# Kernel optimization log

Measured on AMD Instinct MI355X. Metric: run time of the kernel, lower is better.

Reference implementation:

```python
import jax, jax.numpy as jnp
import numpy as np
from jax import lax

EPS = 1e-7  # keras K.epsilon()
DN = ('NHWC', 'HWIO', 'NHWC')


def _box_avg(z, k):
    """Depthwise k x k box filter with SAME padding, scaled by 1/(k*k*C).
    Matches tf.nn.depthwise_conv2d with a ones/(k*k*C) kernel, implemented
    separably (two 1D convs) for efficiency."""
    C = z.shape[-1]
    scale = 1.0 / (k * k * C)  # note: keras code divides by full kernel size incl. C
    kh = jnp.ones((k, 1, 1, C), z.dtype)
    kw = jnp.ones((1, k, 1, C), z.dtype)
    z = lax.conv_general_dilated(z, kh, (1, 1), 'SAME',
                                 dimension_numbers=DN, feature_group_count=C)
    z = lax.conv_general_dilated(z, kw, (1, 1), 'SAME',
                                 dimension_numbers=DN, feature_group_count=C)
    return z * scale


def setup_inputs() -> dict:
    key = jax.random.key(0)
    x = jax.random.normal(key, (8, 1024, 1024, 2), dtype=jnp.float32)
    return {"x": x, "filter_size": 61}


def reference(x, filter_size):
    k = int(filter_size)
    # norm_method == 'std':
    out = x - _box_avg(x, k)                       # local mean-subtract
    c1 = _box_avg(out, k)
    c2 = _box_avg(out * out, k)
    std = jnp.sqrt(c2 - c1 * c1) + EPS             # local window std
    return out / std
```

## Files before the change

### kernel.cpp

```cpp
#include <hip/hip_runtime.h>
#include <math.h>

#define NB 8
#define HH 1024
#define WW 1024
#define CC 2
#define RAD 30
#define KS 61
#define ROWSZ (WW * CC)
#define IMGSZ (HH * ROWSZ)
#define STR4 (ROWSZ / 4)
#define NCOL4 (NB * STR4)
#define VSEGH 32
#define VNSEG (HH / VSEGH)
#define EPSV 1e-7f
#define SCALEV (1.0f / (float)(KS * KS * CC))
#define PDW (WW + WW / 8)
#define PD(i) ((i) + ((i) >> 3))

__device__ __forceinline__ float4 f4add(float4 a, float4 b) {
    return make_float4(a.x + b.x, a.y + b.y, a.z + b.z, a.w + b.w);
}
__device__ __forceinline__ float4 f4sub(float4 a, float4 b) {
    return make_float4(a.x - b.x, a.y - b.y, a.z - b.z, a.w - b.w);
}
__device__ __forceinline__ float4 f4fma(float4 a, float4 b, float4 c) {
    return make_float4(fmaf(a.x, b.x, c.x), fmaf(a.y, b.y, c.y),
                       fmaf(a.z, b.z, c.z), fmaf(a.w, b.w, c.w));
}

__global__ __launch_bounds__(256) void vbox_kernel(const float* __restrict__ in,
                                                   float* __restrict__ out) {
    int tid = blockIdx.x * 256 + threadIdx.x;
    int col = tid & (NCOL4 - 1);
    int seg = tid >> 12;
    int n = col >> 9;
    int w4 = col & (STR4 - 1);
    const float4* ip = (const float4*)(in + (size_t)n * IMGSZ) + w4;
    float4* op = (float4*)(out + (size_t)n * IMGSZ) + w4;
    int h0 = seg * VSEGH;
    float4 S = make_float4(0.f, 0.f, 0.f, 0.f);
    int lo = h0 - RAD; if (lo < 0) lo = 0;
    int hiex = h0 + RAD;
    int h = lo;
    for (; h + 4 <= hiex; h += 4) {
        float4 v0 = ip[(h + 0) * STR4];
        float4 v1 = ip[(h + 1) * STR4];
        float4 v2 = ip[(h + 2) * STR4];
        float4 v3 = ip[(h + 3) * STR4];
        S = f4add(S, f4add(f4add(v0, v1), f4add(v2, v3)));
    }
    for (; h < hiex; ++h) S = f4add(S, ip[h * STR4]);

    if (seg != 0 && seg != VNSEG - 1) {
        for (int ho = h0; ho < h0 + VSEGH; ho += 4) {
            float4 a0 = ip[(ho + 0 + RAD) * STR4];
            float4 a1 = ip[(ho + 1 + RAD) * STR4];
            float4 a2 = ip[(ho + 2 + RAD) * STR4];
            float4 a3 = ip[(ho + 3 + RAD) * STR4];
            float4 b0 = ip[(ho + 0 - RAD) * STR4];
            float4 b1 = ip[(ho + 1 - RAD) * STR4];
            float4 b2 = ip[(ho + 2 - RAD) * STR4];
            float4 b3 = ip[(ho + 3 - RAD) * STR4];
            S = f4add(S, a0); op[(ho + 0) * STR4] = S; S = f4sub(S, b0);
            S = f4add(S, a1); op[(ho + 1) * STR4] = S; S = f4sub(S, b1);
            S = f4add(S, a2); op[(ho + 2) * STR4] = S; S = f4sub(S, b2);
            S = f4add(S, a3); op[(ho + 3) * STR4] = S; S = f4sub(S, b3);
        }
    } else {
        const float4 Z = make_float4(0.f, 0.f, 0.f, 0.f);
        for (int ho = h0; ho < h0 + VSEGH; ho += 4) {
            float4 a[4], b[4];
            #pragma unroll
            for (int i = 0; i < 4; ++i) {
                int ha = ho + i + RAD;
                a[i] = (ha < HH) ? ip[ha * STR4] : Z;
            }
            #pragma unroll
            for (int i = 0; i < 4; ++i) {
                int hb = ho + i - RAD;
                b[i] = (hb >= 0) ? ip[hb * STR4] : Z;
            }
            #pragma unroll
            for (int i = 0; i < 4; ++i) {
                S = f4add(S, a[i]);
                op[(ho + i) * STR4] = S;
                S = f4sub(S, b[i]);
            }
        }
    }
}

__global__ __launch_bounds__(256) void vbox2_kernel(const float* __restrict__ in,
                                                    float* __restrict__ o1,
                                                    float* __restrict__ o2) {
    int tid = blockIdx.x * 256 + threadIdx.x;
    int col = tid & (NCOL4 - 1);
    int seg = tid >> 12;
    int n = col >> 9;
    int w4 = col & (STR4 - 1);
    const float4* ip = (const float4*)(in + (size_t)n * IMGSZ) + w4;
    float4* p1 = (float4*)(o1 + (size_t)n * IMGSZ) + w4;
    float4* p2 = (float4*)(o2 + (size_t)n * IMGSZ) + w4;
    int h0 = seg * VSEGH;
    float4 S = make_float4(0.f, 0.f, 0.f, 0.f);
    float4 Q = make_float4(0.f, 0.f, 0.f, 0.f);
    int lo = h0 - RAD; if (lo < 0) lo = 0;
    int hiex = h0 + RAD;
    int h = lo;
    for (; h + 4 <= hiex; h += 4) {
        float4 v0 = ip[(h + 0) * STR4];
        float4 v1 = ip[(h + 1) * STR4];
        float4 v2 = ip[(h + 2) * STR4];
        float4 v3 = ip[(h + 3) * STR4];
        S = f4add(S, f4add(f4add(v0, v1), f4add(v2, v3)));
        Q = f4fma(v0, v0, Q); Q = f4fma(v1, v1, Q);
        Q = f4fma(v2, v2, Q); Q = f4fma(v3, v3, Q);
    }
    for (; h < hiex; ++h) {
        float4 v = ip[h * STR4];
        S = f4add(S, v); Q = f4fma(v, v, Q);
    }

    if (seg != 0 && seg != VNSEG - 1) {
        for (int ho = h0; ho < h0 + VSEGH; ho += 4) {
            float4 a0 = ip[(ho + 0 + RAD) * STR4];
            float4 a1 = ip[(ho + 1 + RAD) * STR4];
            float4 a2 = ip[(ho + 2 + RAD) * STR4];
            float4 a3 = ip[(ho + 3 + RAD) * STR4];
            float4 b0 = ip[(ho + 0 - RAD) * STR4];
            float4 b1 = ip[(ho + 1 - RAD) * STR4];
            float4 b2 = ip[(ho + 2 - RAD) * STR4];
            float4 b3 = ip[(ho + 3 - RAD) * STR4];
            S = f4add(S, a0); Q = f4fma(a0, a0, Q);
            p1[(ho + 0) * STR4] = S; p2[(ho + 0) * STR4] = Q;
            S = f4sub(S, b0); Q = make_float4(fmaf(-b0.x, b0.x, Q.x), fmaf(-b0.y, b0.y, Q.y), fmaf(-b0.z, b0.z, Q.z), fmaf(-b0.w, b0.w, Q.w));
            S = f4add(S, a1); Q = f4fma(a1, a1, Q);
            p1[(ho + 1) * STR4] = S; p2[(ho + 1) * STR4] = Q;
            S = f4sub(S, b1); Q = make_float4(fmaf(-b1.x, b1.x, Q.x), fmaf(-b1.y, b1.y, Q.y), fmaf(-b1.z, b1.z, Q.z), fmaf(-b1.w, b1.w, Q.w));
            S = f4add(S, a2); Q = f4fma(a2, a2, Q);
            p1[(ho + 2) * STR4] = S; p2[(ho + 2) * STR4] = Q;
            S = f4sub(S, b2); Q = make_float4(fmaf(-b2.x, b2.x, Q.x), fmaf(-b2.y, b2.y, Q.y), fmaf(-b2.z, b2.z, Q.z), fmaf(-b2.w, b2.w, Q.w));
            S = f4add(S, a3); Q = f4fma(a3, a3, Q);
            p1[(ho + 3) * STR4] = S; p2[(ho + 3) * STR4] = Q;
            S = f4sub(S, b3); Q = make_float4(fmaf(-b3.x, b3.x, Q.x), fmaf(-b3.y, b3.y, Q.y), fmaf(-b3.z, b3.z, Q.z), fmaf(-b3.w, b3.w, Q.w));
        }
    } else {
        const float4 Z = make_float4(0.f, 0.f, 0.f, 0.f);
        for (int ho = h0; ho < h0 + VSEGH; ho += 4) {
            float4 a[4], b[4];
            #pragma unroll
            for (int i = 0; i < 4; ++i) {
                int ha = ho + i + RAD;
                a[i] = (ha < HH) ? ip[ha * STR4] : Z;
            }
            #pragma unroll
            for (int i = 0; i < 4; ++i) {
                int hb = ho + i - RAD;
                b[i] = (hb >= 0) ? ip[hb * STR4] : Z;
            }
            #pragma unroll
            for (int i = 0; i < 4; ++i) {
                S = f4add(S, a[i]); Q = f4fma(a[i], a[i], Q);
                p1[(ho + i) * STR4] = S; p2[(ho + i) * STR4] = Q;
                S = f4sub(S, b[i]);
                Q = make_float4(fmaf(-b[i].x, b[i].x, Q.x), fmaf(-b[i].y, b[i].y, Q.y),
                                fmaf(-b[i].z, b[i].z, Q.z), fmaf(-b[i].w, b[i].w, Q.w));
            }
        }
    }
}

__device__ inline float wave_incl_scan(float v) {
    int lane = threadIdx.x & 63;
    #pragma unroll
    for (int d = 1; d < 64; d <<= 1) {
        float o = __shfl_up(v, d, 64);
        if (lane >= d) v += o;
    }
    return v;
}

__global__ __launch_bounds__(256) void hbox_sub_kernel(const float* __restrict__ vsum,
                                                       const float* __restrict__ x,
                                                       float* __restrict__ out) {
    __shared__ float ch[2][PDW];
    __shared__ float wtot[4];
    int t = threadIdx.x;
    size_t g = (size_t)blockIdx.x * ROWSZ;
    const float4* vrow = (const float4*)(vsum + g);
    #pragma unroll
    for (int i = 0; i < 2; ++i) {
        int j = t + 256 * i;
        float4 v = vrow[j];
        ch[0][PD(2 * j)] = v.x;     ch[1][PD(2 * j)] = v.y;
        ch[0][PD(2 * j + 1)] = v.z; ch[1][PD(2 * j + 1)] = v.w;
    }
    __syncthreads();
    int c = t >> 7, j = t & 127, base = j * 8;
    float v[8]; float run = 0.f;
    #pragma unroll
    for (int i = 0; i < 8; ++i) { run += ch[c][PD(base + i)]; v[i] = run; }
    float incl = wave_incl_scan(run);
    int wid = t >> 6;
    if ((t & 63) == 63) wtot[wid] = incl;
    __syncthreads();
    float off = incl - run;
    if (wid & 1) off += wtot[wid - 1];
    #pragma unroll
    for (int i = 0; i < 8; ++i) ch[c][PD(base + i)] = off + v[i];
    __syncthreads();
    const float4* xrow = (const float4*)(x + g);
    float4* orow = (float4*)(out + g);
    #pragma unroll
    for (int i = 0; i < 2; ++i) {
        int jj = t + 256 * i;
        int w0 = 2 * jj, w1 = 2 * jj + 1;
        int hi0 = w0 + RAD; if (hi0 > WW - 1) hi0 = WW - 1;
        int hi1 = w1 + RAD; if (hi1 > WW - 1) hi1 = WW - 1;
        int lo0 = w0 - RAD - 1, lo1 = w1 - RAD - 1;
        float s00 = ch[0][PD(hi0)], s10 = ch[1][PD(hi0)];
        if (lo0 >= 0) { s00 -= ch[0][PD(lo0)]; s10 -= ch[1][PD(lo0)]; }
        float s01 = ch[0][PD(hi1)], s11 = ch[1][PD(hi1)];
        if (lo1 >= 0) { s01 -= ch[0][PD(lo1)]; s11 -= ch[1][PD(lo1)]; }
        float4 xv = xrow[jj];
        float4 o;
        o.x = xv.x - SCALEV * s00; o.y = xv.y - SCALEV * s10;
        o.z = xv.z - SCALEV * s01; o.w = xv.w - SCALEV * s11;
        orow[jj] = o;
    }
}

__global__ __launch_bounds__(256) void hbox_final_kernel(const float* __restrict__ s1v,
                                                         const float* __restrict__ s2v,
                                                         float* __restrict__ out) {
    __shared__ float ch[4][PDW];
    int t = threadIdx.x;
    size_t g = (size_t)blockIdx.x * ROWSZ;
    const float4* arow = (const float4*)(s1v + g);
    const float4* brow = (const float4*)(s2v + g);
    #pragma unroll
    for (int i = 0; i < 2; ++i) {
        int j = t + 256 * i;
        float4 a = arow[j];
        ch[0][PD(2 * j)] = a.x;     ch[1][PD(2 * j)] = a.y;
        ch[0][PD(2 * j + 1)] = a.z; ch[1][PD(2 * j + 1)] = a.w;
        float4 b = brow[j];
        ch[2][PD(2 * j)] = b.x;     ch[3][PD(2 * j)] = b.y;
        ch[2][PD(2 * j + 1)] = b.z; ch[3][PD(2 * j + 1)] = b.w;
    }
    __syncthreads();
    int a = t >> 6, j = t & 63, base = j * 16;
    float v[16]; float run = 0.f;
    #pragma unroll
    for (int i = 0; i < 16; ++i) { run += ch[a][PD(base + i)]; v[i] = run; }
    float incl = wave_incl_scan(run);
    float off = incl - run;
    #pragma unroll
    for (int i = 0; i < 16; ++i) ch[a][PD(base + i)] = off + v[i];
    __syncthreads();
    float4* orow = (float4*)(out + g);
    #pragma unroll
    for (int i = 0; i < 2; ++i) {
        int jj = t + 256 * i;
        int w0 = 2 * jj, w1 = 2 * jj + 1;
        int hi0 = w0 + RAD; if (hi0 > WW - 1) hi0 = WW - 1;
        int hi1 = w1 + RAD; if (hi1 > WW - 1) hi1 = WW - 1;
        int lo0 = w0 - RAD - 1, lo1 = w1 - RAD - 1;
        float s1a = ch[0][PD(hi0)], s1b = ch[1][PD(hi0)];
        float s2a = ch[2][PD(hi0)], s2b = ch[3][PD(hi0)];
        if (lo0 >= 0) {
            s1a -= ch[0][PD(lo0)]; s1b -= ch[1][PD(lo0)];
            s2a -= ch[2][PD(lo0)]; s2b -= ch[3][PD(lo0)];
        }
        float s1c = ch[0][PD(hi1)], s1d = ch[1][PD(hi1)];
        float s2c = ch[2][PD(hi1)], s2d = ch[3][PD(hi1)];
        if (lo1 >= 0) {
            s1c -= ch[0][PD(lo1)]; s1d -= ch[1][PD(lo1)];
            s2c -= ch[2][PD(lo1)]; s2d -= ch[3][PD(lo1)];
        }
        float4 ov = orow[jj];
        float c1, c2, var;
        float4 r;
        c1 = SCALEV * s1a; c2 = SCALEV * s2a; var = c2 - c1 * c1;
        r.x = ov.x / (sqrtf(fmaxf(var, 0.f)) + EPSV);
        c1 = SCALEV * s1b; c2 = SCALEV * s2b; var = c2 - c1 * c1;
        r.y = ov.y / (sqrtf(fmaxf(var, 0.f)) + EPSV);
        c1 = SCALEV * s1c; c2 = SCALEV * s2c; var = c2 - c1 * c1;
        r.z = ov.z / (sqrtf(fmaxf(var, 0.f)) + EPSV);
        c1 = SCALEV * s1d; c2 = SCALEV * s2d; var = c2 - c1 * c1;
        r.w = ov.w / (sqrtf(fmaxf(var, 0.f)) + EPSV);
        orow[jj] = r;
    }
}

extern "C" void kernel_launch(void* const* d_in, const int* in_sizes, int n_in,
                              void* d_out, int out_size, void* d_ws, size_t ws_size,
                              hipStream_t stream) {
    const float* x = (const float*)d_in[0];
    float* out = (float*)d_out;
    float* wsf = (float*)d_ws;
    float* V1 = wsf;
    float* V3 = wsf + (size_t)NB * IMGSZ;

    vbox_kernel<<<(NCOL4 * VNSEG) / 256, 256, 0, stream>>>(x, V1);
    hbox_sub_kernel<<<NB * HH, 256, 0, stream>>>(V1, x, out);
    vbox2_kernel<<<(NCOL4 * VNSEG) / 256, 256, 0, stream>>>(out, V1, V3);
    hbox_final_kernel<<<NB * HH, 256, 0, stream>>>(V1, V3, out);
}
```

Baseline: 251.7 us.

## Fuse horizontal box passes and move second vertical box into final normalization

Reorders the separable filters so the second stage does the horizontal box sums of both out and out² in the same block that computes out, writing horizontal sums to workspace. A new vertical kernel then box-sums those and applies the std normalization directly, removing one kernel and the separate final pass. It also adds software prefetching of the next rows in the vertical loops and sets launch bounds occupancy hints. The trade-off is extra global writes of two horizontal-sum buffers and two streams read in the vertical pass.

```diff
diff --git a/kernel.cpp b/kernel.cpp
--- a/kernel.cpp
+++ b/kernel.cpp
@@ -4,17 +4,16 @@
 #define NB 8
 #define HH 1024
 #define WW 1024
-#define CC 2
 #define RAD 30
 #define KS 61
-#define ROWSZ (WW * CC)
+#define ROWSZ 2048
 #define IMGSZ (HH * ROWSZ)
-#define STR4 (ROWSZ / 4)
+#define STR4 512
 #define NCOL4 (NB * STR4)
 #define VSEGH 32
 #define VNSEG (HH / VSEGH)
 #define EPSV 1e-7f
-#define SCALEV (1.0f / (float)(KS * KS * CC))
+#define SCALEV (1.0f / (float)(KS * KS * 2))
 #define PDW (WW + WW / 8)
 #define PD(i) ((i) + ((i) >> 3))
 
@@ -24,13 +23,9 @@
 __device__ __forceinline__ float4 f4sub(float4 a, float4 b) {
     return make_float4(a.x - b.x, a.y - b.y, a.z - b.z, a.w - b.w);
 }
-__device__ __forceinline__ float4 f4fma(float4 a, float4 b, float4 c) {
-    return make_float4(fmaf(a.x, b.x, c.x), fmaf(a.y, b.y, c.y),
-                       fmaf(a.z, b.z, c.z), fmaf(a.w, b.w, c.w));
-}
-
-__global__ __launch_bounds__(256) void vbox_kernel(const float* __restrict__ in,
-                                                   float* __restrict__ out) {
+
+__global__ __launch_bounds__(256, 2) void vbox_kernel(const float* __restrict__ in,
+                                                      float* __restrict__ out) {
     int tid = blockIdx.x * 256 + threadIdx.x;
     int col = tid & (NCOL4 - 1);
     int seg = tid >> 12;
@@ -38,38 +33,43 @@
     int w4 = col & (STR4 - 1);
     const float4* ip = (const float4*)(in + (size_t)n * IMGSZ) + w4;
     float4* op = (float4*)(out + (size_t)n * IMGSZ) + w4;
-    int h0 = seg * VSEGH;
+    int h0 = seg * VSEGH, hend = h0 + VSEGH;
     float4 S = make_float4(0.f, 0.f, 0.f, 0.f);
     int lo = h0 - RAD; if (lo < 0) lo = 0;
-    int hiex = h0 + RAD;
     int h = lo;
-    for (; h + 4 <= hiex; h += 4) {
+    for (; h + 4 <= h0 + RAD; h += 4) {
         float4 v0 = ip[(h + 0) * STR4];
         float4 v1 = ip[(h + 1) * STR4];
         float4 v2 = ip[(h + 2) * STR4];
         float4 v3 = ip[(h + 3) * STR4];
         S = f4add(S, f4add(f4add(v0, v1), f4add(v2, v3)));
     }
-    for (; h < hiex; ++h) S = f4add(S, ip[h * STR4]);
+    for (; h < h0 + RAD; ++h) S = f4add(S, ip[h * STR4]);
 
     if (seg != 0 && seg != VNSEG - 1) {
-        for (int ho = h0; ho < h0 + VSEGH; ho += 4) {
-            float4 a0 = ip[(ho + 0 + RAD) * STR4];
-            float4 a1 = ip[(ho + 1 + RAD) * STR4];
-            float4 a2 = ip[(ho + 2 + RAD) * STR4];
-            float4 a3 = ip[(ho + 3 + RAD) * STR4];
-            float4 b0 = ip[(ho + 0 - RAD) * STR4];
-            float4 b1 = ip[(ho + 1 - RAD) * STR4];
-            float4 b2 = ip[(ho + 2 - RAD) * STR4];
-            float4 b3 = ip[(ho + 3 - RAD) * STR4];
-            S = f4add(S, a0); op[(ho + 0) * STR4] = S; S = f4sub(S, b0);
-            S = f4add(S, a1); op[(ho + 1) * STR4] = S; S = f4sub(S, b1);
-            S = f4add(S, a2); op[(ho + 2) * STR4] = S; S = f4sub(S, b2);
-            S = f4add(S, a3); op[(ho + 3) * STR4] = S; S = f4sub(S, b3);
+        const float4* lp = ip + (h0 + RAD) * STR4;
+        const float4* tp = ip + (h0 - RAD) * STR4;
+        float4* sp = op + h0 * STR4;
+        float4 A[4], B[4];
+        #pragma unroll
+        for (int i = 0; i < 4; ++i) { A[i] = lp[i * STR4]; B[i] = tp[i * STR4]; }
+        for (int ho = h0; ho < hend; ho += 4) {
+            int noff = (ho + 4 < hend) ? (ho + 4 - h0) * STR4 : 0;
+            float4 An[4], Bn[4];
+            #pragma unroll
+            for (int i = 0; i < 4; ++i) { An[i] = lp[noff + i * STR4]; Bn[i] = tp[noff + i * STR4]; }
+            #pragma unroll
+            for (int i = 0; i < 4; ++i) {
+                S = f4add(S, A[i]);
+                sp[(ho - h0 + i) * STR4] = S;
+                S = f4sub(S, B[i]);
+            }
+            #pragma unroll
+            for (int i = 0; i < 4; ++i) { A[i] = An[i]; B[i] = Bn[i]; }
         }
     } else {
         const float4 Z = make_float4(0.f, 0.f, 0.f, 0.f);
-        for (int ho = h0; ho < h0 + VSEGH; ho += 4) {
+        for (int ho = h0; ho < hend; ho += 4) {
             float4 a[4], b[4];
             #pragma unroll
             for (int i = 0; i < 4; ++i) {
@@ -86,86 +86,6 @@
                 S = f4add(S, a[i]);
                 op[(ho + i) * STR4] = S;
                 S = f4sub(S, b[i]);
-            }
-        }
-    }
-}
-
-__global__ __launch_bounds__(256) void vbox2_kernel(const float* __restrict__ in,
-                                                    float* __restrict__ o1,
-                                                    float* __restrict__ o2) {
-    int tid = blockIdx.x * 256 + threadIdx.x;
-    int col = tid & (NCOL4 - 1);
-    int seg = tid >> 12;
-    int n = col >> 9;
-    int w4 = col & (STR4 - 1);
-    const float4* ip = (const float4*)(in + (size_t)n * IMGSZ) + w4;
-    float4* p1 = (float4*)(o1 + (size_t)n * IMGSZ) + w4;
-    float4* p2 = (float4*)(o2 + (size_t)n * IMGSZ) + w4;
-    int h0 = seg * VSEGH;
-    float4 S = make_float4(0.f, 0.f, 0.f, 0.f);
-    float4 Q = make_float4(0.f, 0.f, 0.f, 0.f);
-    int lo = h0 - RAD; if (lo < 0) lo = 0;
-    int hiex = h0 + RAD;
-    int h = lo;
-    for (; h + 4 <= hiex; h += 4) {
-        float4 v0 = ip[(h + 0) * STR4];
-        float4 v1 = ip[(h + 1) * STR4];
-        float4 v2 = ip[(h + 2) * STR4];
-        float4 v3 = ip[(h + 3) * STR4];
-        S = f4add(S, f4add(f4add(v0, v1), f4add(v2, v3)));
-        Q = f4fma(v0, v0, Q); Q = f4fma(v1, v1, Q);
-        Q = f4fma(v2, v2, Q); Q = f4fma(v3, v3, Q);
-    }
-    for (; h < hiex; ++h) {
-        float4 v = ip[h * STR4];
-        S = f4add(S, v); Q = f4fma(v, v, Q);
-    }
-
-    if (seg != 0 && seg != VNSEG - 1) {
-        for (int ho = h0; ho < h0 + VSEGH; ho += 4) {
-            float4 a0 = ip[(ho + 0 + RAD) * STR4];
-            float4 a1 = ip[(ho + 1 + RAD) * STR4];
-            float4 a2 = ip[(ho + 2 + RAD) * STR4];
-            float4 a3 = ip[(ho + 3 + RAD) * STR4];
-            float4 b0 = ip[(ho + 0 - RAD) * STR4];
-            float4 b1 = ip[(ho + 1 - RAD) * STR4];
-            float4 b2 = ip[(ho + 2 - RAD) * STR4];
-            float4 b3 = ip[(ho + 3 - RAD) * STR4];
-            S = f4add(S, a0); Q = f4fma(a0, a0, Q);
-            p1[(ho + 0) * STR4] = S; p2[(ho + 0) * STR4] = Q;
-            S = f4sub(S, b0); Q = make_float4(fmaf(-b0.x, b0.x, Q.x), fmaf(-b0.y, b0.y, Q.y), fmaf(-b0.z, b0.z, Q.z), fmaf(-b0.w, b0.w, Q.w));
-            S = f4add(S, a1); Q = f4fma(a1, a1, Q);
-            p1[(ho + 1) * STR4] = S; p2[(ho + 1) * STR4] = Q;
-            S = f4sub(S, b1); Q = make_float4(fmaf(-b1.x, b1.x, Q.x), fmaf(-b1.y, b1.y, Q.y), fmaf(-b1.z, b1.z, Q.z), fmaf(-b1.w, b1.w, Q.w));
-            S = f4add(S, a2); Q = f4fma(a2, a2, Q);
-            p1[(ho + 2) * STR4] = S; p2[(ho + 2) * STR4] = Q;
-            S = f4sub(S, b2); Q = make_float4(fmaf(-b2.x, b2.x, Q.x), fmaf(-b2.y, b2.y, Q.y), fmaf(-b2.z, b2.z, Q.z), fmaf(-b2.w, b2.w, Q.w));
-            S = f4add(S, a3); Q = f4fma(a3, a3, Q);
-            p1[(ho + 3) * STR4] = S; p2[(ho + 3) * STR4] = Q;
-            S = f4sub(S, b3); Q = make_float4(fmaf(-b3.x, b3.x, Q.x), fmaf(-b3.y, b3.y, Q.y), fmaf(-b3.z, b3.z, Q.z), fmaf(-b3.w, b3.w, Q.w));
-        }
-    } else {
-        const float4 Z = make_float4(0.f, 0.f, 0.f, 0.f);
-        for (int ho = h0; ho < h0 + VSEGH; ho += 4) {
-            float4 a[4], b[4];
-            #pragma unroll
-            for (int i = 0; i < 4; ++i) {
-                int ha = ho + i + RAD;
-                a[i] = (ha < HH) ? ip[ha * STR4] : Z;
-            }
-            #pragma unroll
-            for (int i = 0; i < 4; ++i) {
-                int hb = ho + i - RAD;
-                b[i] = (hb >= 0) ? ip[hb * STR4] : Z;
-            }
-            #pragma unroll
-            for (int i = 0; i < 4; ++i) {
-                S = f4add(S, a[i]); Q = f4fma(a[i], a[i], Q);
-                p1[(ho + i) * STR4] = S; p2[(ho + i) * STR4] = Q;
-                S = f4sub(S, b[i]);
-                Q = make_float4(fmaf(-b[i].x, b[i].x, Q.x), fmaf(-b[i].y, b[i].y, Q.y),
-                                fmaf(-b[i].z, b[i].z, Q.z), fmaf(-b[i].w, b[i].w, Q.w));
             }
         }
     }
@@ -181,41 +101,42 @@
     return v;
 }
 
-__global__ __launch_bounds__(256) void hbox_sub_kernel(const float* __restrict__ vsum,
-                                                       const float* __restrict__ x,
-                                                       float* __restrict__ out) {
-    __shared__ float ch[2][PDW];
+__global__ __launch_bounds__(256) void hboxq_kernel(float* v1q1,
+                                                    const float* __restrict__ x,
+                                                    float* __restrict__ outp,
+                                                    float* __restrict__ q2) {
+    __shared__ float ch[4][PDW];
     __shared__ float wtot[4];
     int t = threadIdx.x;
+    int t2 = t + 256;
     size_t g = (size_t)blockIdx.x * ROWSZ;
-    const float4* vrow = (const float4*)(vsum + g);
-    #pragma unroll
-    for (int i = 0; i < 2; ++i) {
-        int j = t + 256 * i;
-        float4 v = vrow[j];
-        ch[0][PD(2 * j)] = v.x;     ch[1][PD(2 * j)] = v.y;
-        ch[0][PD(2 * j + 1)] = v.z; ch[1][PD(2 * j + 1)] = v.w;
-    }
-    __syncthreads();
-    int c = t >> 7, j = t & 127, base = j * 8;
-    float v[8]; float run = 0.f;
-    #pragma unroll
-    for (int i = 0; i < 8; ++i) { run += ch[c][PD(base + i)]; v[i] = run; }
-    float incl = wave_incl_scan(run);
-    int wid = t >> 6;
-    if ((t & 63) == 63) wtot[wid] = incl;
-    __syncthreads();
-    float off = incl - run;
-    if (wid & 1) off += wtot[wid - 1];
-    #pragma unroll
-    for (int i = 0; i < 8; ++i) ch[c][PD(base + i)] = off + v[i];
-    __syncthreads();
+    const float4* vrow = (const float4*)(v1q1 + g);
     const float4* xrow = (const float4*)(x + g);
-    float4* orow = (float4*)(out + g);
-    #pragma unroll
-    for (int i = 0; i < 2; ++i) {
-        int jj = t + 256 * i;
-        int w0 = 2 * jj, w1 = 2 * jj + 1;
+    float4 va = vrow[t], vb = vrow[t2];
+    float4 xa = xrow[t], xb = xrow[t2];
+    ch[0][PD(2 * t)] = va.x;      ch[1][PD(2 * t)] = va.y;
+    ch[0][PD(2 * t + 1)] = va.z;  ch[1][PD(2 * t + 1)] = va.w;
+    ch[0][PD(2 * t2)] = vb.x;     ch[1][PD(2 * t2)] = vb.y;
+    ch[0][PD(2 * t2 + 1)] = vb.z; ch[1][PD(2 * t2 + 1)] = vb.w;
+    __syncthreads();
+    {
+        int c = t >> 7, j = t & 127, base = j * 8;
+        float v[8]; float run = 0.f;
+        #pragma unroll
+        for (int i = 0; i < 8; ++i) { run += ch[c][PD(base + i)]; v[i] = run; }
+        float incl = wave_incl_scan(run);
+        int wid = t >> 6;
+        if ((t & 63) == 63) wtot[wid] = incl;
+        __syncthreads();
+        float off = incl - run;
+        if (wid & 1) off += wtot[wid - 1];
+        #pragma unroll
+        for (int i = 0; i < 8; ++i) ch[c][PD(base + i)] = off + v[i];
+    }
+    __syncthreads();
+    float4 o0, o1;
+    {
+        int w0 = 2 * t, w1 = 2 * t + 1;
         int hi0 = w0 + RAD; if (hi0 > WW - 1) hi0 = WW - 1;
         int hi1 = w1 + RAD; if (hi1 > WW - 1) hi1 = WW - 1;
         int lo0 = w0 - RAD - 1, lo1 = w1 - RAD - 1;
@@ -223,74 +144,167 @@
         if (lo0 >= 0) { s00 -= ch[0][PD(lo0)]; s10 -= ch[1][PD(lo0)]; }
         float s01 = ch[0][PD(hi1)], s11 = ch[1][PD(hi1)];
         if (lo1 >= 0) { s01 -= ch[0][PD(lo1)]; s11 -= ch[1][PD(lo1)]; }
-        float4 xv = xrow[jj];
-        float4 o;
-        o.x = xv.x - SCALEV * s00; o.y = xv.y - SCALEV * s10;
-        o.z = xv.z - SCALEV * s01; o.w = xv.w - SCALEV * s11;
-        orow[jj] = o;
-    }
-}
-
-__global__ __launch_bounds__(256) void hbox_final_kernel(const float* __restrict__ s1v,
-                                                         const float* __restrict__ s2v,
-                                                         float* __restrict__ out) {
-    __shared__ float ch[4][PDW];
-    int t = threadIdx.x;
-    size_t g = (size_t)blockIdx.x * ROWSZ;
-    const float4* arow = (const float4*)(s1v + g);
-    const float4* brow = (const float4*)(s2v + g);
+        o0 = make_float4(xa.x - SCALEV * s00, xa.y - SCALEV * s10,
+                         xa.z - SCALEV * s01, xa.w - SCALEV * s11);
+        w0 = 2 * t2; w1 = 2 * t2 + 1;
+        hi0 = w0 + RAD; if (hi0 > WW - 1) hi0 = WW - 1;
+        hi1 = w1 + RAD; if (hi1 > WW - 1) hi1 = WW - 1;
+        lo0 = w0 - RAD - 1; lo1 = w1 - RAD - 1;
+        s00 = ch[0][PD(hi0)]; s10 = ch[1][PD(hi0)];
+        if (lo0 >= 0) { s00 -= ch[0][PD(lo0)]; s10 -= ch[1][PD(lo0)]; }
+        s01 = ch[0][PD(hi1)]; s11 = ch[1][PD(hi1)];
+        if (lo1 >= 0) { s01 -= ch[0][PD(lo1)]; s11 -= ch[1][PD(lo1)]; }
+        o1 = make_float4(xb.x - SCALEV * s00, xb.y - SCALEV * s10,
+                         xb.z - SCALEV * s01, xb.w - SCALEV * s11);
+    }
+    float4* orow = (float4*)(outp + g);
+    orow[t] = o0; orow[t2] = o1;
+    __syncthreads();
+    ch[0][PD(2 * t)] = o0.x;          ch[1][PD(2 * t)] = o0.y;
+    ch[0][PD(2 * t + 1)] = o0.z;      ch[1][PD(2 * t + 1)] = o0.w;
+    ch[2][PD(2 * t)] = o0.x * o0.x;   ch[3][PD(2 * t)] = o0.y * o0.y;
+    ch[2][PD(2 * t + 1)] = o0.z * o0.z; ch[3][PD(2 * t + 1)] = o0.w * o0.w;
+    ch[0][PD(2 * t2)] = o1.x;         ch[1][PD(2 * t2)] = o1.y;
+    ch[0][PD(2 * t2 + 1)] = o1.z;     ch[1][PD(2 * t2 + 1)] = o1.w;
+    ch[2][PD(2 * t2)] = o1.x * o1.x;  ch[3][PD(2 * t2)] = o1.y * o1.y;
+    ch[2][PD(2 * t2 + 1)] = o1.z * o1.z; ch[3][PD(2 * t2 + 1)] = o1.w * o1.w;
+    __syncthreads();
+    {
+        int a = t >> 6, j = t & 63, base = j * 16;
+        float v[16]; float run = 0.f;
+        #pragma unroll
+        for (int i = 0; i < 16; ++i) { run += ch[a][PD(base + i)]; v[i] = run; }
+        float incl = wave_incl_scan(run);
+        float off = incl - run;
+        #pragma unroll
+        for (int i = 0; i < 16; ++i) ch[a][PD(base + i)] = off + v[i];
+    }
+    __syncthreads();
+    float4* q1row = (float4*)(v1q1 + g);
+    float4* q2row = (float4*)(q2 + g);
     #pragma unroll
-    for (int i = 0; i < 2; ++i) {
-        int j = t + 256 * i;
-        float4 a = arow[j];
-        ch[0][PD(2 * j)] = a.x;     ch[1][PD(2 * j)] = a.y;
-        ch[0][PD(2 * j + 1)] = a.z; ch[1][PD(2 * j + 1)] = a.w;
-        float4 b = brow[j];
-        ch[2][PD(2 * j)] = b.x;     ch[3][PD(2 * j)] = b.y;
-        ch[2][PD(2 * j + 1)] = b.z; ch[3][PD(2 * j + 1)] = b.w;
-    }
-    __syncthreads();
-    int a = t >> 6, j = t & 63, base = j * 16;
-    float v[16]; float run = 0.f;
-    #pragma unroll
-    for (int i = 0; i < 16; ++i) { run += ch[a][PD(base + i)]; v[i] = run; }
-    float incl = wave_incl_scan(run);
-    float off = incl - run;
-    #pragma unroll
-    for (int i = 0; i < 16; ++i) ch[a][PD(base + i)] = off + v[i];
-    __syncthreads();
-    float4* orow = (float4*)(out + g);
-    #pragma unroll
-    for (int i = 0; i < 2; ++i) {
-        int jj = t + 256 * i;
+    for (int k = 0; k < 2; ++k) {
+        int jj = (k == 0) ? t : t2;
         int w0 = 2 * jj, w1 = 2 * jj + 1;
         int hi0 = w0 + RAD; if (hi0 > WW - 1) hi0 = WW - 1;
         int hi1 = w1 + RAD; if (hi1 > WW - 1) hi1 = WW - 1;
         int lo0 = w0 - RAD - 1, lo1 = w1 - RAD - 1;
-        float s1a = ch[0][PD(hi0)], s1b = ch[1][PD(hi0)];
-        float s2a = ch[2][PD(hi0)], s2b = ch[3][PD(hi0)];
+        float a0 = ch[0][PD(hi0)], b0 = ch[1][PD(hi0)];
+        float c0 = ch[2][PD(hi0)], d0 = ch[3][PD(hi0)];
         if (lo0 >= 0) {
-            s1a -= ch[0][PD(lo0)]; s1b -= ch[1][PD(lo0)];
-            s2a -= ch[2][PD(lo0)]; s2b -= ch[3][PD(lo0)];
-        }
-        float s1c = ch[0][PD(hi1)], s1d = ch[1][PD(hi1)];
-        float s2c = ch[2][PD(hi1)], s2d = ch[3][PD(hi1)];
+            a0 -= ch[0][PD(lo0)]; b0 -= ch[1][PD(lo0)];
+            c0 -= ch[2][PD(lo0)]; d0 -= ch[3][PD(lo0)];
+        }
+        float a1 = ch[0][PD(hi1)], b1 = ch[1][PD(hi1)];
+        float c1v = ch[2][PD(hi1)], d1 = ch[3][PD(hi1)];
         if (lo1 >= 0) {
-            s1c -= ch[0][PD(lo1)]; s1d -= ch[1][PD(lo1)];
-            s2c -= ch[2][PD(lo1)]; s2d -= ch[3][PD(lo1)];
-        }
-        float4 ov = orow[jj];
-        float c1, c2, var;
-        float4 r;
-        c1 = SCALEV * s1a; c2 = SCALEV * s2a; var = c2 - c1 * c1;
-        r.x = ov.x / (sqrtf(fmaxf(var, 0.f)) + EPSV);
-        c1 = SCALEV * s1b; c2 = SCALEV * s2b; var = c2 - c1 * c1;
-        r.y = ov.y / (sqrtf(fmaxf(var, 0.f)) + EPSV);
-        c1 = SCALEV * s1c; c2 = SCALEV * s2c; var = c2 - c1 * c1;
-        r.z = ov.z / (sqrtf(fmaxf(var, 0.f)) + EPSV);
-        c1 = SCALEV * s1d; c2 = SCALEV * s2d; var = c2 - c1 * c1;
-        r.w = ov.w / (sqrtf(fmaxf(var, 0.f)) + EPSV);
-        orow[jj] = r;
+            a1 -= ch[0][PD(lo1)]; b1 -= ch[1][PD(lo1)];
+            c1v -= ch[2][PD(lo1)]; d1 -= ch[3][PD(lo1)];
+        }
+        q1row[jj] = make_float4(a0, b0, a1, b1);
+        q2row[jj] = make_float4(c0, d0, c1v, d1);
+    }
+}
+
+__device__ __forceinline__ float4 fin4(float4 S1, float4 S2, float4 O) {
+    float4 r;
+    float c1, var;
+    c1 = SCALEV * S1.x; var = SCALEV * S2.x - c1 * c1;
+    r.x = O.x / (sqrtf(fmaxf(var, 0.f)) + EPSV);
+    c1 = SCALEV * S1.y; var = SCALEV * S2.y - c1 * c1;
+    r.y = O.y / (sqrtf(fmaxf(var, 0.f)) + EPSV);
+    c1 = SCALEV * S1.z; var = SCALEV * S2.z - c1 * c1;
+    r.z = O.z / (sqrtf(fmaxf(var, 0.f)) + EPSV);
+    c1 = SCALEV * S1.w; var = SCALEV * S2.w - c1 * c1;
+    r.w = O.w / (sqrtf(fmaxf(var, 0.f)) + EPSV);
+    return r;
+}
+
+__global__ __launch_bounds__(256, 2) void vfin_kernel(const float* __restrict__ q1g,
+                                                      const float* __restrict__ q2g,
+                                                      float* __restrict__ outg) {
+    int tid = blockIdx.x * 256 + threadIdx.x;
+    int col = tid & (NCOL4 - 1);
+    int seg = tid >> 12;
+    int n = col >> 9;
+    int w4 = col & (STR4 - 1);
+    const float4* p1 = (const float4*)(q1g + (size_t)n * IMGSZ) + w4;
+    const float4* p2 = (const float4*)(q2g + (size_t)n * IMGSZ) + w4;
+    float4* po = (float4*)(outg + (size_t)n * IMGSZ) + w4;
+    int h0 = seg * VSEGH, hend = h0 + VSEGH;
+    float4 S1 = make_float4(0.f, 0.f, 0.f, 0.f);
+    float4 S2 = make_float4(0.f, 0.f, 0.f, 0.f);
+    int lo = h0 - RAD; if (lo < 0) lo = 0;
+    int h = lo;
+    for (; h + 2 <= h0 + RAD; h += 2) {
+        float4 a0 = p1[(h + 0) * STR4], a1 = p1[(h + 1) * STR4];
+        float4 b0 = p2[(h + 0) * STR4], b1 = p2[(h + 1) * STR4];
+        S1 = f4add(S1, f4add(a0, a1));
+        S2 = f4add(S2, f4add(b0, b1));
+    }
+    for (; h < h0 + RAD; ++h) {
+        S1 = f4add(S1, p1[h * STR4]);
+        S2 = f4add(S2, p2[h * STR4]);
+    }
+
+    if (seg != 0 && seg != VNSEG - 1) {
+        const float4* lp1 = p1 + (h0 + RAD) * STR4;
+        const float4* tp1 = p1 + (h0 - RAD) * STR4;
+        const float4* lp2 = p2 + (h0 + RAD) * STR4;
+        const float4* tp2 = p2 + (h0 - RAD) * STR4;
+        float4* cp = po + h0 * STR4;
+        float4 L1[2], L2[2], T1[2], T2[2], O[2];
+        #pragma unroll
+        for (int i = 0; i < 2; ++i) {
+            L1[i] = lp1[i * STR4]; L2[i] = lp2[i * STR4];
+            T1[i] = tp1[i * STR4]; T2[i] = tp2[i * STR4];
+            O[i] = cp[i * STR4];
+        }
+        for (int ho = h0; ho < hend; ho += 2) {
+            int noff = (ho + 2 < hend) ? (ho + 2 - h0) * STR4 : 0;
+            float4 L1n[2], L2n[2], T1n[2], T2n[2], On[2];
+            #pragma unroll
+            for (int i = 0; i < 2; ++i) {
+                L1n[i] = lp1[noff + i * STR4]; L2n[i] = lp2[noff + i * STR4];
+                T1n[i] = tp1[noff + i * STR4]; T2n[i] = tp2[noff + i * STR4];
+                On[i] = cp[noff + i * STR4];
+            }
+            #pragma unroll
+            for (int i = 0; i < 2; ++i) {
+                S1 = f4add(S1, L1[i]); S2 = f4add(S2, L2[i]);
+                cp[(ho - h0 + i) * STR4] = fin4(S1, S2, O[i]);
+                S1 = f4sub(S1, T1[i]); S2 = f4sub(S2, T2[i]);
+            }
+            #pragma unroll
+            for (int i = 0; i < 2; ++i) {
+                L1[i] = L1n[i]; L2[i] = L2n[i];
+                T1[i] = T1n[i]; T2[i] = T2n[i]; O[i] = On[i];
+            }
+        }
+    } else {
+        const float4 Z = make_float4(0.f, 0.f, 0.f, 0.f);
+        for (int ho = h0; ho < hend; ho += 2) {
+            float4 a1[2], a2[2], b1[2], b2[2], O[2];
+            #pragma unroll
+            for (int i = 0; i < 2; ++i) {
+                int ha = ho + i + RAD;
+                a1[i] = (ha < HH) ? p1[ha * STR4] : Z;
+                a2[i] = (ha < HH) ? p2[ha * STR4] : Z;
+                O[i] = po[(ho + i) * STR4];
+            }
+            #pragma unroll
+            for (int i = 0; i < 2; ++i) {
+                int hb = ho + i - RAD;
+                b1[i] = (hb >= 0) ? p1[hb * STR4] : Z;
+                b2[i] = (hb >= 0) ? p2[hb * STR4] : Z;
+            }
+            #pragma unroll
+            for (int i = 0; i < 2; ++i) {
+                S1 = f4add(S1, a1[i]); S2 = f4add(S2, a2[i]);
+                po[(ho + i) * STR4] = fin4(S1, S2, O[i]);
+                S1 = f4sub(S1, b1[i]); S2 = f4sub(S2, b2[i]);
+            }
+        }
     }
 }
 
@@ -299,12 +313,10 @@
                               hipStream_t stream) {
     const float* x = (const float*)d_in[0];
     float* out = (float*)d_out;
-    float* wsf = (float*)d_ws;
-    float* V1 = wsf;
-    float* V3 = wsf + (size_t)NB * IMGSZ;
+    float* V1 = (float*)d_ws;
+    float* Q2 = V1 + (size_t)NB * IMGSZ;
 
     vbox_kernel<<<(NCOL4 * VNSEG) / 256, 256, 0, stream>>>(x, V1);
-    hbox_sub_kernel<<<NB * HH, 256, 0, stream>>>(V1, x, out);
-    vbox2_kernel<<<(NCOL4 * VNSEG) / 256, 256, 0, stream>>>(out, V1, V3);
-    hbox_final_kernel<<<NB * HH, 256, 0, stream>>>(V1, V3, out);
-}
+    hboxq_kernel<<<NB * HH, 256, 0, stream>>>(V1, x, out, Q2);
+    vfin_kernel<<<(NCOL4 * VNSEG) / 256, 256, 0, stream>>>(V1, Q2, out);
+}
```

Measured after the change: 263.3 us. 4.6% more time.

## Store vertical box-sum intermediates as packed bf16 and use float2 columns

Applied to the files above, without the earlier changes.

The vertical box-sum kernels now write their intermediate column sums as bf16 pairs packed into 32-bit words, halving the intermediate buffer traffic. The horizontal kernels unpack these with shifts. Each thread now handles a float2 column instead of a float4, which doubles the thread count, and the interior loops unroll by 8. Rounding the running sums, including the sum of squares used for the variance, to bf16 loses a lot of precision and risks errors or cancellation in c2 - c1*c1.

```diff
diff --git a/kernel.cpp b/kernel.cpp
--- a/kernel.cpp
+++ b/kernel.cpp
@@ -4,168 +4,179 @@
 #define NB 8
 #define HH 1024
 #define WW 1024
-#define CC 2
 #define RAD 30
 #define KS 61
-#define ROWSZ (WW * CC)
+#define ROWSZ 2048
 #define IMGSZ (HH * ROWSZ)
-#define STR4 (ROWSZ / 4)
-#define NCOL4 (NB * STR4)
+#define STR2 1024
+#define NCOL2 (NB * STR2)
 #define VSEGH 32
 #define VNSEG (HH / VSEGH)
 #define EPSV 1e-7f
-#define SCALEV (1.0f / (float)(KS * KS * CC))
+#define SCALEV (1.0f / (float)(KS * KS * 2))
 #define PDW (WW + WW / 8)
 #define PD(i) ((i) + ((i) >> 3))
 
-__device__ __forceinline__ float4 f4add(float4 a, float4 b) {
-    return make_float4(a.x + b.x, a.y + b.y, a.z + b.z, a.w + b.w);
-}
-__device__ __forceinline__ float4 f4sub(float4 a, float4 b) {
-    return make_float4(a.x - b.x, a.y - b.y, a.z - b.z, a.w - b.w);
-}
-__device__ __forceinline__ float4 f4fma(float4 a, float4 b, float4 c) {
-    return make_float4(fmaf(a.x, b.x, c.x), fmaf(a.y, b.y, c.y),
-                       fmaf(a.z, b.z, c.z), fmaf(a.w, b.w, c.w));
-}
-
-__global__ __launch_bounds__(256) void vbox_kernel(const float* __restrict__ in,
-                                                   float* __restrict__ out) {
+__device__ __forceinline__ unsigned bf16_rn(float f) {
+    unsigned u = __float_as_uint(f);
+    return (u + 0x7FFFu + ((u >> 16) & 1u)) >> 16;
+}
+__device__ __forceinline__ unsigned pk2(float a, float b) {
+    return bf16_rn(a) | (bf16_rn(b) << 16);
+}
+__device__ __forceinline__ float2 up2(unsigned u) {
+    return make_float2(__uint_as_float(u << 16),
+                       __uint_as_float(u & 0xFFFF0000u));
+}
+
+__device__ __forceinline__ float2 f2add(float2 a, float2 b) {
+    return make_float2(a.x + b.x, a.y + b.y);
+}
+__device__ __forceinline__ float2 f2sub(float2 a, float2 b) {
+    return make_float2(a.x - b.x, a.y - b.y);
+}
+
+__global__ __launch_bounds__(256, 4) void vbox_kernel(const float* __restrict__ in,
+                                                      unsigned* __restrict__ out) {
     int tid = blockIdx.x * 256 + threadIdx.x;
-    int col = tid & (NCOL4 - 1);
-    int seg = tid >> 12;
-    int n = col >> 9;
-    int w4 = col & (STR4 - 1);
-    const float4* ip = (const float4*)(in + (size_t)n * IMGSZ) + w4;
-    float4* op = (float4*)(out + (size_t)n * IMGSZ) + w4;
+    int col = tid & (NCOL2 - 1);
+    int seg = tid >> 13;
+    int n = col >> 10;
+    int w2 = col & (STR2 - 1);
+    const float2* ip = (const float2*)(in + (size_t)n * IMGSZ) + w2;
+    unsigned* op = out + (size_t)n * (IMGSZ / 2) + w2;
     int h0 = seg * VSEGH;
-    float4 S = make_float4(0.f, 0.f, 0.f, 0.f);
+    float2 S = make_float2(0.f, 0.f);
     int lo = h0 - RAD; if (lo < 0) lo = 0;
-    int hiex = h0 + RAD;
     int h = lo;
-    for (; h + 4 <= hiex; h += 4) {
-        float4 v0 = ip[(h + 0) * STR4];
-        float4 v1 = ip[(h + 1) * STR4];
-        float4 v2 = ip[(h + 2) * STR4];
-        float4 v3 = ip[(h + 3) * STR4];
-        S = f4add(S, f4add(f4add(v0, v1), f4add(v2, v3)));
-    }
-    for (; h < hiex; ++h) S = f4add(S, ip[h * STR4]);
+    for (; h + 4 <= h0 + RAD; h += 4) {
+        float2 v0 = ip[(h + 0) * STR2];
+        float2 v1 = ip[(h + 1) * STR2];
+        float2 v2 = ip[(h + 2) * STR2];
+        float2 v3 = ip[(h + 3) * STR2];
+        S = f2add(S, f2add(f2add(v0, v1), f2add(v2, v3)));
+    }
+    for (; h < h0 + RAD; ++h) S = f2add(S, ip[h * STR2]);
 
     if (seg != 0 && seg != VNSEG - 1) {
+        const float2* lp = ip + (h0 + RAD) * STR2;
+        const float2* tp = ip + (h0 - RAD) * STR2;
+        unsigned* opp = op + (size_t)h0 * STR2;
+        for (int r = 0; r < VSEGH; r += 8) {
+            float2 L[8], T[8];
+            #pragma unroll
+            for (int i = 0; i < 8; ++i) L[i] = lp[(r + i) * STR2];
+            #pragma unroll
+            for (int i = 0; i < 8; ++i) T[i] = tp[(r + i) * STR2];
+            #pragma unroll
+            for (int i = 0; i < 8; ++i) {
+                S = f2add(S, L[i]);
+                opp[(r + i) * STR2] = pk2(S.x, S.y);
+                S = f2sub(S, T[i]);
+            }
+        }
+    } else {
+        const float2 Z = make_float2(0.f, 0.f);
         for (int ho = h0; ho < h0 + VSEGH; ho += 4) {
-            float4 a0 = ip[(ho + 0 + RAD) * STR4];
-            float4 a1 = ip[(ho + 1 + RAD) * STR4];
-            float4 a2 = ip[(ho + 2 + RAD) * STR4];
-            float4 a3 = ip[(ho + 3 + RAD) * STR4];
-            float4 b0 = ip[(ho + 0 - RAD) * STR4];
-            float4 b1 = ip[(ho + 1 - RAD) * STR4];
-            float4 b2 = ip[(ho + 2 - RAD) * STR4];
-            float4 b3 = ip[(ho + 3 - RAD) * STR4];
-            S = f4add(S, a0); op[(ho + 0) * STR4] = S; S = f4sub(S, b0);
-            S = f4add(S, a1); op[(ho + 1) * STR4] = S; S = f4sub(S, b1);
-            S = f4add(S, a2); op[(ho + 2) * STR4] = S; S = f4sub(S, b2);
-            S = f4add(S, a3); op[(ho + 3) * STR4] = S; S = f4sub(S, b3);
+            float2 a[4], b[4];
+            #pragma unroll
+            for (int i = 0; i < 4; ++i) {
+                int ha = ho + i + RAD;
+                a[i] = (ha < HH) ? ip[ha * STR2] : Z;
+            }
+            #pragma unroll
+            for (int i = 0; i < 4; ++i) {
+                int hb = ho + i - RAD;
+                b[i] = (hb >= 0) ? ip[hb * STR2] : Z;
+            }
+            #pragma unroll
+            for (int i = 0; i < 4; ++i) {
+                S = f2add(S, a[i]);
+                op[(size_t)(ho + i) * STR2] = pk2(S.x, S.y);
+                S = f2sub(S, b[i]);
+            }
+        }
+    }
+}
+
+__global__ __launch_bounds__(256, 4) void vbox2_kernel(const float* __restrict__ in,
+                                                       unsigned* __restrict__ o1,
+                                                       unsigned* __restrict__ o2) {
+    int tid = blockIdx.x * 256 + threadIdx.x;
+    int col = tid & (NCOL2 - 1);
+    int seg = tid >> 13;
+    int n = col >> 10;
+    int w2 = col & (STR2 - 1);
+    const float2* ip = (const float2*)(in + (size_t)n * IMGSZ) + w2;
+    unsigned* p1 = o1 + (size_t)n * (IMGSZ / 2) + w2;
+    unsigned* p2 = o2 + (size_t)n * (IMGSZ / 2) + w2;
+    int h0 = seg * VSEGH;
+    float2 S = make_float2(0.f, 0.f);
+    float2 Q = make_float2(0.f, 0.f);
+    int lo = h0 - RAD; if (lo < 0) lo = 0;
+    int h = lo;
+    for (; h + 4 <= h0 + RAD; h += 4) {
+        float2 v0 = ip[(h + 0) * STR2];
+        float2 v1 = ip[(h + 1) * STR2];
+        float2 v2 = ip[(h + 2) * STR2];
+        float2 v3 = ip[(h + 3) * STR2];
+        S = f2add(S, f2add(f2add(v0, v1), f2add(v2, v3)));
+        Q.x = fmaf(v0.x, v0.x, fmaf(v1.x, v1.x, fmaf(v2.x, v2.x, fmaf(v3.x, v3.x, Q.x))));
+        Q.y = fmaf(v0.y, v0.y, fmaf(v1.y, v1.y, fmaf(v2.y, v2.y, fmaf(v3.y, v3.y, Q.y))));
+    }
+    for (; h < h0 + RAD; ++h) {
+        float2 v = ip[h * STR2];
+        S = f2add(S, v);
+        Q.x = fmaf(v.x, v.x, Q.x); Q.y = fmaf(v.y, v.y, Q.y);
+    }
+
+    if (seg != 0 && seg != VNSEG - 1) {
+        const float2* lp = ip + (h0 + RAD) * STR2;
+        const float2* tp = ip + (h0 - RAD) * STR2;
+        unsigned* q1 = p1 + (size_t)h0 * STR2;
+        unsigned* q2 = p2 + (size_t)h0 * STR2;
+        for (int r = 0; r < VSEGH; r += 8) {
+            float2 L[8], T[8];
+            #pragma unroll
+            for (int i = 0; i < 8; ++i) L[i] = lp[(r + i) * STR2];
+            #pragma unroll
+            for (int i = 0; i < 8; ++i) T[i] = tp[(r + i) * STR2];
+            #pragma unroll
+            for (int i = 0; i < 8; ++i) {
+                S = f2add(S, L[i]);
+                Q.x = fmaf(L[i].x, L[i].x, Q.x);
+                Q.y = fmaf(L[i].y, L[i].y, Q.y);
+                q1[(r + i) * STR2] = pk2(S.x, S.y);
+                q2[(r + i) * STR2] = pk2(Q.x, Q.y);
+                S = f2sub(S, T[i]);
+                Q.x = fmaf(-T[i].x, T[i].x, Q.x);
+                Q.y = fmaf(-T[i].y, T[i].y, Q.y);
+            }
         }
     } else {
-        const float4 Z = make_float4(0.f, 0.f, 0.f, 0.f);
+        const float2 Z = make_float2(0.f, 0.f);
         for (int ho = h0; ho < h0 + VSEGH; ho += 4) {
-            float4 a[4], b[4];
+            float2 a[4], b[4];
             #pragma unroll
             for (int i = 0; i < 4; ++i) {
                 int ha = ho + i + RAD;
-                a[i] = (ha < HH) ? ip[ha * STR4] : Z;
+                a[i] = (ha < HH) ? ip[ha * STR2] : Z;
             }
             #pragma unroll
             for (int i = 0; i < 4; ++i) {
                 int hb = ho + i - RAD;
-                b[i] = (hb >= 0) ? ip[hb * STR4] : Z;
-            }
-            #pragma unroll
-            for (int i = 0; i < 4; ++i) {
-                S = f4add(S, a[i]);
-                op[(ho + i) * STR4] = S;
-                S = f4sub(S, b[i]);
-            }
-        }
-    }
-}
-
-__global__ __launch_bounds__(256) void vbox2_kernel(const float* __restrict__ in,
-                                                    float* __restrict__ o1,
-                                                    float* __restrict__ o2) {
-    int tid = blockIdx.x * 256 + threadIdx.x;
-    int col = tid & (NCOL4 - 1);
-    int seg = tid >> 12;
-    int n = col >> 9;
-    int w4 = col & (STR4 - 1);
-    const float4* ip = (const float4*)(in + (size_t)n * IMGSZ) + w4;
-    float4* p1 = (float4*)(o1 + (size_t)n * IMGSZ) + w4;
-    float4* p2 = (float4*)(o2 + (size_t)n * IMGSZ) + w4;
-    int h0 = seg * VSEGH;
-    float4 S = make_float4(0.f, 0.f, 0.f, 0.f);
-    float4 Q = make_float4(0.f, 0.f, 0.f, 0.f);
-    int lo = h0 - RAD; if (lo < 0) lo = 0;
-    int hiex = h0 + RAD;
-    int h = lo;
-    for (; h + 4 <= hiex; h += 4) {
-        float4 v0 = ip[(h + 0) * STR4];
-        float4 v1 = ip[(h + 1) * STR4];
-        float4 v2 = ip[(h + 2) * STR4];
-        float4 v3 = ip[(h + 3) * STR4];
-        S = f4add(S, f4add(f4add(v0, v1), f4add(v2, v3)));
-        Q = f4fma(v0, v0, Q); Q = f4fma(v1, v1, Q);
-        Q = f4fma(v2, v2, Q); Q = f4fma(v3, v3, Q);
-    }
-    for (; h < hiex; ++h) {
-        float4 v = ip[h * STR4];
-        S = f4add(S, v); Q = f4fma(v, v, Q);
-    }
-
-    if (seg != 0 && seg != VNSEG - 1) {
-        for (int ho = h0; ho < h0 + VSEGH; ho += 4) {
-            float4 a0 = ip[(ho + 0 + RAD) * STR4];
-            float4 a1 = ip[(ho + 1 + RAD) * STR4];
-            float4 a2 = ip[(ho + 2 + RAD) * STR4];
-            float4 a3 = ip[(ho + 3 + RAD) * STR4];
-            float4 b0 = ip[(ho + 0 - RAD) * STR4];
-            float4 b1 = ip[(ho + 1 - RAD) * STR4];
-            float4 b2 = ip[(ho + 2 - RAD) * STR4];
-            float4 b3 = ip[(ho + 3 - RAD) * STR4];
-            S = f4add(S, a0); Q = f4fma(a0, a0, Q);
-            p1[(ho + 0) * STR4] = S; p2[(ho + 0) * STR4] = Q;
-            S = f4sub(S, b0); Q = make_float4(fmaf(-b0.x, b0.x, Q.x), fmaf(-b0.y, b0.y, Q.y), fmaf(-b0.z, b0.z, Q.z), fmaf(-b0.w, b0.w, Q.w));
-            S = f4add(S, a1); Q = f4fma(a1, a1, Q);
-            p1[(ho + 1) * STR4] = S; p2[(ho + 1) * STR4] = Q;
-            S = f4sub(S, b1); Q = make_float4(fmaf(-b1.x, b1.x, Q.x), fmaf(-b1.y, b1.y, Q.y), fmaf(-b1.z, b1.z, Q.z), fmaf(-b1.w, b1.w, Q.w));
-            S = f4add(S, a2); Q = f4fma(a2, a2, Q);
-            p1[(ho + 2) * STR4] = S; p2[(ho + 2) * STR4] = Q;
-            S = f4sub(S, b2); Q = make_float4(fmaf(-b2.x, b2.x, Q.x), fmaf(-b2.y, b2.y, Q.y), fmaf(-b2.z, b2.z, Q.z), fmaf(-b2.w, b2.w, Q.w));
-            S = f4add(S, a3); Q = f4fma(a3, a3, Q);
-            p1[(ho + 3) * STR4] = S; p2[(ho + 3) * STR4] = Q;
-            S = f4sub(S, b3); Q = make_float4(fmaf(-b3.x, b3.x, Q.x), fmaf(-b3.y, b3.y, Q.y), fmaf(-b3.z, b3.z, Q.z), fmaf(-b3.w, b3.w, Q.w));
-        }
-    } else {
-        const float4 Z = make_float4(0.f, 0.f, 0.f, 0.f);
-        for (int ho = h0; ho < h0 + VSEGH; ho += 4) {
-            float4 a[4], b[4];
-            #pragma unroll
-            for (int i = 0; i < 4; ++i) {
-                int ha = ho + i + RAD;
-                a[i] = (ha < HH) ? ip[ha * STR4] : Z;
-            }
-            #pragma unroll
-            for (int i = 0; i < 4; ++i) {
-                int hb = ho + i - RAD;
-                b[i] = (hb >= 0) ? ip[hb * STR4] : Z;
-            }
-            #pragma unroll
-            for (int i = 0; i < 4; ++i) {
-                S = f4add(S, a[i]); Q = f4fma(a[i], a[i], Q);
-                p1[(ho + i) * STR4] = S; p2[(ho + i) * STR4] = Q;
-                S = f4sub(S, b[i]);
-                Q = make_float4(fmaf(-b[i].x, b[i].x, Q.x), fmaf(-b[i].y, b[i].y, Q.y),
-                                fmaf(-b[i].z, b[i].z, Q.z), fmaf(-b[i].w, b[i].w, Q.w));
+                b[i] = (hb >= 0) ? ip[hb * STR2] : Z;
+            }
+            #pragma unroll
+            for (int i = 0; i < 4; ++i) {
+                S = f2add(S, a[i]);
+                Q.x = fmaf(a[i].x, a[i].x, Q.x);
+                Q.y = fmaf(a[i].y, a[i].y, Q.y);
+                p1[(size_t)(ho + i) * STR2] = pk2(S.x, S.y);
+                p2[(size_t)(ho + i) * STR2] = pk2(Q.x, Q.y);
+                S = f2sub(S, b[i]);
+                Q.x = fmaf(-b[i].x, b[i].x, Q.x);
+                Q.y = fmaf(-b[i].y, b[i].y, Q.y);
             }
         }
     }
@@ -181,34 +192,38 @@
     return v;
 }
 
-__global__ __launch_bounds__(256) void hbox_sub_kernel(const float* __restrict__ vsum,
+__global__ __launch_bounds__(256) void hbox_sub_kernel(const unsigned* __restrict__ vsum,
                                                        const float* __restrict__ x,
                                                        float* __restrict__ out) {
     __shared__ float ch[2][PDW];
     __shared__ float wtot[4];
     int t = threadIdx.x;
     size_t g = (size_t)blockIdx.x * ROWSZ;
-    const float4* vrow = (const float4*)(vsum + g);
-    #pragma unroll
-    for (int i = 0; i < 2; ++i) {
-        int j = t + 256 * i;
-        float4 v = vrow[j];
-        ch[0][PD(2 * j)] = v.x;     ch[1][PD(2 * j)] = v.y;
-        ch[0][PD(2 * j + 1)] = v.z; ch[1][PD(2 * j + 1)] = v.w;
+    const uint4* vrow = (const uint4*)(vsum + (size_t)blockIdx.x * STR2);
+    uint4 u = vrow[t];
+    {
+        float2 p0 = up2(u.x), p1 = up2(u.y), p2 = up2(u.z), p3 = up2(u.w);
+        int w = 4 * t;
+        ch[0][PD(w + 0)] = p0.x; ch[1][PD(w + 0)] = p0.y;
+        ch[0][PD(w + 1)] = p1.x; ch[1][PD(w + 1)] = p1.y;
+        ch[0][PD(w + 2)] = p2.x; ch[1][PD(w + 2)] = p2.y;
+        ch[0][PD(w + 3)] = p3.x; ch[1][PD(w + 3)] = p3.y;
     }
     __syncthreads();
-    int c = t >> 7, j = t & 127, base = j * 8;
-    float v[8]; float run = 0.f;
-    #pragma unroll
-    for (int i = 0; i < 8; ++i) { run += ch[c][PD(base + i)]; v[i] = run; }
-    float incl = wave_incl_scan(run);
-    int wid = t >> 6;
-    if ((t & 63) == 63) wtot[wid] = incl;
-    __syncthreads();
-    float off = incl - run;
-    if (wid & 1) off += wtot[wid - 1];
-    #pragma unroll
-    for (int i = 0; i < 8; ++i) ch[c][PD(base + i)] = off + v[i];
+    {
+        int c = t >> 7, j = t & 127, base = j * 8;
+        float v[8]; float run = 0.f;
+        #pragma unroll
+        for (int i = 0; i < 8; ++i) { run += ch[c][PD(base + i)]; v[i] = run; }
+        float incl = wave_incl_scan(run);
+        int wid = t >> 6;
+        if ((t & 63) == 63) wtot[wid] = incl;
+        __syncthreads();
+        float off = incl - run;
+        if (wid & 1) off += wtot[wid - 1];
+        #pragma unroll
+        for (int i = 0; i < 8; ++i) ch[c][PD(base + i)] = off + v[i];
+    }
     __syncthreads();
     const float4* xrow = (const float4*)(x + g);
     float4* orow = (float4*)(out + g);
@@ -231,33 +246,39 @@
     }
 }
 
-__global__ __launch_bounds__(256) void hbox_final_kernel(const float* __restrict__ s1v,
-                                                         const float* __restrict__ s2v,
+__global__ __launch_bounds__(256) void hbox_final_kernel(const unsigned* __restrict__ z1,
+                                                         const unsigned* __restrict__ z2,
                                                          float* __restrict__ out) {
     __shared__ float ch[4][PDW];
     int t = threadIdx.x;
     size_t g = (size_t)blockIdx.x * ROWSZ;
-    const float4* arow = (const float4*)(s1v + g);
-    const float4* brow = (const float4*)(s2v + g);
-    #pragma unroll
-    for (int i = 0; i < 2; ++i) {
-        int j = t + 256 * i;
-        float4 a = arow[j];
-        ch[0][PD(2 * j)] = a.x;     ch[1][PD(2 * j)] = a.y;
-        ch[0][PD(2 * j + 1)] = a.z; ch[1][PD(2 * j + 1)] = a.w;
-        float4 b = brow[j];
-        ch[2][PD(2 * j)] = b.x;     ch[3][PD(2 * j)] = b.y;
-        ch[2][PD(2 * j + 1)] = b.z; ch[3][PD(2 * j + 1)] = b.w;
+    const uint4* arow = (const uint4*)(z1 + (size_t)blockIdx.x * STR2);
+    const uint4* brow = (const uint4*)(z2 + (size_t)blockIdx.x * STR2);
+    uint4 ua = arow[t], ub = brow[t];
+    {
+        float2 p0 = up2(ua.x), p1 = up2(ua.y), p2 = up2(ua.z), p3 = up2(ua.w);
+        float2 q0 = up2(ub.x), q1 = up2(ub.y), q2 = up2(ub.z), q3 = up2(ub.w);
+        int w = 4 * t;
+        ch[0][PD(w + 0)] = p0.x; ch[1][PD(w + 0)] = p0.y;
+        ch[0][PD(w + 1)] = p1.x; ch[1][PD(w + 1)] = p1.y;
+        ch[0][PD(w + 2)] = p2.x; ch[1][PD(w + 2)] = p2.y;
+        ch[0][PD(w + 3)] = p3.x; ch[1][PD(w + 3)] = p3.y;
+        ch[2][PD(w + 0)] = q0.x; ch[3][PD(w + 0)] = q0.y;
+        ch[2][PD(w + 1)] = q1.x; ch[3][PD(w + 1)] = q1.y;
+        ch[2][PD(w + 2)] = q2.x; ch[3][PD(w + 2)] = q2.y;
+        ch[2][PD(w + 3)] = q3.x; ch[3][PD(w + 3)] = q3.y;
     }
     __syncthreads();
-    int a = t >> 6, j = t & 63, base = j * 16;
-    float v[16]; float run = 0.f;
-    #pragma unroll
-    for (int i = 0; i < 16; ++i) { run += ch[a][PD(base + i)]; v[i] = run; }
-    float incl = wave_incl_scan(run);
-    float off = incl - run;
-    #pragma unroll
-    for (int i = 0; i < 16; ++i) ch[a][PD(base + i)] = off + v[i];
+    {
+        int a = t >> 6, j = t & 63, base = j * 16;
+        float v[16]; float run = 0.f;
+        #pragma unroll
+        for (int i = 0; i < 16; ++i) { run += ch[a][PD(base + i)]; v[i] = run; }
+        float incl = wave_incl_scan(run);
+        float off = incl - run;
+        #pragma unroll
+        for (int i = 0; i < 16; ++i) ch[a][PD(base + i)] = off + v[i];
+    }
     __syncthreads();
     float4* orow = (float4*)(out + g);
     #pragma unroll
@@ -299,12 +320,13 @@
                               hipStream_t stream) {
     const float* x = (const float*)d_in[0];
     float* out = (float*)d_out;
-    float* wsf = (float*)d_ws;
-    float* V1 = wsf;
-    float* V3 = wsf + (size_t)NB * IMGSZ;
-
-    vbox_kernel<<<(NCOL4 * VNSEG) / 256, 256, 0, stream>>>(x, V1);
+    unsigned* V1 = (unsigned*)d_ws;
+    unsigned* Z1 = V1 + (size_t)NB * IMGSZ / 2;
+    unsigned* Z2 = Z1 + (size_t)NB * IMGSZ / 2;
+
+    int vgrid = (NCOL2 * VNSEG) / 256;
+    vbox_kernel<<<vgrid, 256, 0, stream>>>(x, V1);
     hbox_sub_kernel<<<NB * HH, 256, 0, stream>>>(V1, x, out);
-    vbox2_kernel<<<(NCOL4 * VNSEG) / 256, 256, 0, stream>>>(out, V1, V3);
-    hbox_final_kernel<<<NB * HH, 256, 0, stream>>>(V1, V3, out);
-}
+    vbox2_kernel<<<vgrid, 256, 0, stream>>>(out, Z1, Z2);
+    hbox_final_kernel<<<NB * HH, 256, 0, stream>>>(Z1, Z2, out);
+}
```

After: 219.0 us. 13.0% less time.
